# Kernel optimization log

Hardware: AMD Instinct MI355X
Metric: run time of the kernel (lower is better)

Reference implementation:

```python
import jax, jax.numpy as jnp
import numpy as np


def setup_inputs() -> dict:
    key = jax.random.key(0)
    k1, k2 = jax.random.split(key)
    B, C, T = 8, 64, 65536  # batch, channels, sequence length (power of 2)
    x = jax.random.normal(k1, (B, C, T), dtype=jnp.float32)
    h = jax.random.normal(k2, (B, C, T), dtype=jnp.float32)
    return {"x": x, "h": h}


def reference(x, h):
    """Causal (linear) convolution of x with kernel h via FFT, truncated to
    the input length — the math computed by FlashFFTConv. The original module
    casts the signal x to bfloat16 before the conv (kernel h stays fp32); we
    mimic that quantization, then compute the FFT in fp32."""
    T = x.shape[-1]
    n = 2 * T  # zero-pad to 2T so circular conv == linear causal conv on [0, T)
    xb = x.astype(jnp.bfloat16).astype(jnp.float32)  # bf16 quantization of signal
    X = jnp.fft.rfft(xb, n=n)          # (B, C, T+1) complex64
    H = jnp.fft.rfft(h, n=n)           # (B, C, T+1) complex64
    y = jnp.fft.irfft(X * H, n=n)[..., :T]  # causal output, same length as x
    return y.astype(jnp.float32)
```

## Files before the change

### kernel.cpp

```cpp
#include <hip/hip_runtime.h>
#include <hip/hip_bf16.h>
#include <hip/hip_fp16.h>
#include <math.h>


#define TLEN 65536
#define NFFT 131072
#define NN1 512
#define NN2 256

#define WFENCE() asm volatile("s_waitcnt lgkmcnt(0)" ::: "memory")

typedef float cpx __attribute__((ext_vector_type(2)));

static __device__ __forceinline__ cpx mkc(float a, float b) { cpx r; r.x = a; r.y = b; return r; }
static __device__ __forceinline__ cpx h2c(__half2 h) { float2 f = __half22float2(h); return mkc(f.x, f.y); }
static __device__ __forceinline__ __half2 c2h(cpx c) { return __float22half2_rn(make_float2(c.x, c.y)); }

static __device__ __forceinline__ cpx cadd(cpx a, cpx b) {
  cpx d; asm("v_pk_add_f32 %0, %1, %2" : "=v"(d) : "v"(a), "v"(b)); return d;
}
static __device__ __forceinline__ cpx csub(cpx a, cpx b) {
  cpx d; asm("v_pk_add_f32 %0, %1, %2 neg_lo:[0,1] neg_hi:[0,1]" : "=v"(d) : "v"(a), "v"(b)); return d;
}
static __device__ __forceinline__ cpx cscale(cpx a, cpx c) {
  cpx d; asm("v_pk_mul_f32 %0, %1, %2" : "=v"(d) : "v"(a), "v"(c)); return d;
}
static __device__ __forceinline__ cpx cmul(cpx a, cpx b) {
  cpx t, d;
  asm("v_pk_mul_f32 %0, %1, %2 op_sel:[0,0] op_sel_hi:[0,1]" : "=v"(t) : "v"(a), "v"(b));
  asm("v_pk_fma_f32 %0, %1, %2, %3 op_sel:[1,1,0] op_sel_hi:[1,0,1] neg_lo:[1,0,0]"
      : "=v"(d) : "v"(a), "v"(b), "v"(t));
  return d;
}
static __device__ __forceinline__ cpx cmulc(cpx a, cpx b) {
  cpx t, d;
  asm("v_pk_mul_f32 %0, %1, %2 op_sel:[0,0] op_sel_hi:[0,1]" : "=v"(t) : "v"(a), "v"(b));
  asm("v_pk_fma_f32 %0, %1, %2, %3 op_sel:[1,1,0] op_sel_hi:[1,0,1] neg_hi:[0,0,1]"
      : "=v"(d) : "v"(a), "v"(b), "v"(t));
  return d;
}
template <int S> static __device__ __forceinline__ cpx cmuli(cpx a) {
  cpx z = mkc(0.f, 0.f); cpx d;
  if constexpr (S == 1)
    asm("v_pk_add_f32 %0, %1, %2 op_sel:[1,0] op_sel_hi:[0,0] neg_lo:[1,0]" : "=v"(d) : "v"(a), "v"(z));
  else
    asm("v_pk_add_f32 %0, %1, %2 op_sel:[1,0] op_sel_hi:[0,0] neg_hi:[1,0]" : "=v"(d) : "v"(a), "v"(z));
  return d;
}
template <int S> static __device__ __forceinline__ cpx cw1(cpx d, cpx Cc) {
  cpx u;
  if constexpr (S == -1)
    asm("v_pk_add_f32 %0, %1, %1 op_sel:[0,1] op_sel_hi:[1,0] neg_hi:[0,1]" : "=v"(u) : "v"(d));
  else
    asm("v_pk_add_f32 %0, %1, %1 op_sel:[0,1] op_sel_hi:[0,1] neg_lo:[0,1]" : "=v"(u) : "v"(d));
  return cscale(u, Cc);
}
template <int S> static __device__ __forceinline__ cpx cw3(cpx d, cpx Cc) {
  cpx u;
  if constexpr (S == -1)
    asm("v_pk_add_f32 %0, %1, %1 op_sel:[1,0] op_sel_hi:[0,1] neg_lo:[0,1] neg_hi:[1,1]" : "=v"(u) : "v"(d));
  else
    asm("v_pk_add_f32 %0, %1, %1 op_sel:[0,1] op_sel_hi:[0,1] neg_lo:[1,1] neg_hi:[0,1]" : "=v"(u) : "v"(d));
  return cscale(u, Cc);
}

template <int S>
__device__ __forceinline__ void fft8(cpx v[8]) {
  cpx Cc; Cc.x = 0.70710678118654752f; Cc.y = 0.70710678118654752f;
  cpx b0 = cadd(v[0], v[4]), b4 = csub(v[0], v[4]);
  cpx b1 = cadd(v[1], v[5]), d1 = csub(v[1], v[5]);
  cpx b2 = cadd(v[2], v[6]), d2 = csub(v[2], v[6]);
  cpx b3 = cadd(v[3], v[7]), d3 = csub(v[3], v[7]);
  cpx b5 = cw1<S>(d1, Cc);
  cpx b6 = cmuli<S>(d2);
  cpx b7 = cw3<S>(d3, Cc);
  cpx c0 = cadd(b0, b2), c2 = csub(b0, b2);
  cpx c1 = cadd(b1, b3), e3 = csub(b1, b3);
  cpx c3 = cmuli<S>(e3);
  cpx c4 = cadd(b4, b6), c6 = csub(b4, b6);
  cpx c5 = cadd(b5, b7), e7 = csub(b5, b7);
  cpx c7 = cmuli<S>(e7);
  v[0] = cadd(c0, c1); v[4] = csub(c0, c1);
  v[2] = cadd(c2, c3); v[6] = csub(c2, c3);
  v[1] = cadd(c4, c5); v[5] = csub(c4, c5);
  v[3] = cadd(c6, c7); v[7] = csub(c6, c7);
}

template <int S>
__device__ __forceinline__ void fft4(cpx v[4]) {
  cpx t0 = cadd(v[0], v[2]), t1 = csub(v[0], v[2]);
  cpx t2 = cadd(v[1], v[3]), t3 = csub(v[1], v[3]);
  cpx it3 = cmuli<S>(t3);
  v[0] = cadd(t0, t2); v[2] = csub(t0, t2);
  v[1] = cadd(t1, it3); v[3] = csub(t1, it3);
}

__global__ void k_init_tw(cpx* __restrict__ tw) {
  int m = blockIdx.x * 256 + threadIdx.x;
  double ang = (double)m * (-2.0 * 3.14159265358979323846 / (double)NFFT);
  tw[m] = mkc((float)cos(ang), (float)sin(ang));
}

__global__ __launch_bounds__(256, 3) void k_fwd_inner(
    const float* __restrict__ x, const float* __restrict__ h,
    __half2* __restrict__ buf, const cpx* __restrict__ tw) {
  __shared__ __half2 tz[128 * 18];
  __shared__ cpx xch[4 * 512];
  __shared__ __half2 to[256 * 17];
  __shared__ cpx w256[256];
  const int tid = threadIdx.x;
  const int lane = tid & 63;
  const int wid = tid >> 6;
  const int s = blockIdx.x >> 5;
  const int n1b = (blockIdx.x & 31) * 16;
  w256[tid] = tw[tid * (NFFT / 256)];
  const float* xp = x + (size_t)s * TLEN;
  const float* hp = h + (size_t)s * TLEN;
  {
    int a = tid & 3, q = tid >> 2;
#pragma unroll
    for (int iter = 0; iter < 2; ++iter) {
      int n2 = q + 64 * iter;
      size_t gi = (size_t)(n1b + 4 * a) + (size_t)512 * n2;
      float4 xv = *(const float4*)(xp + gi);
      float4 hv = *(const float4*)(hp + gi);
      float xs[4] = {xv.x, xv.y, xv.z, xv.w};
      float hs[4] = {hv.x, hv.y, hv.z, hv.w};
#pragma unroll
      for (int c = 0; c < 4; ++c) {
        float xb = __bfloat162float(__float2bfloat16(xs[c]));
        tz[18 * n2 + 4 * a + c] = __float22half2_rn(make_float2(xb, hs[c]));
      }
    }
  }
  __syncthreads();
  cpx* X = xch + wid * 512;
  const int f = lane >> 5;
  const int l5 = lane & 31;
  const int fb = f * 256;
  const int hh = l5 >> 2, bb = l5 & 3;
#pragma unroll
  for (int p2 = 0; p2 < 2; ++p2) {
    const int n1l = 8 * p2 + 2 * wid + f;
    const int n1 = n1b + n1l;
    cpx tbase = tw[n1 * (hh + 8 * bb)];
    cpx tstep = tw[32 * n1];
    cpx v[8];
#pragma unroll
    for (int j = 0; j < 4; ++j) v[j] = h2c(tz[18 * (32 * j + l5) + n1l]);
#pragma unroll
    for (int j = 4; j < 8; ++j) v[j] = mkc(0.f, 0.f);
    fft8<-1>(v);
    { cpx w1 = w256[l5]; cpx pw = w1;
#pragma unroll
      for (int k0 = 1; k0 < 8; ++k0) { v[k0] = cmul(v[k0], pw); pw = cmul(pw, w1); } }
#pragma unroll
    for (int k0 = 0; k0 < 8; ++k0) X[fb + 32 * k0 + (l5 ^ (4 * k0))] = v[k0];
    WFENCE();
#pragma unroll
    for (int j2 = 0; j2 < 8; ++j2) v[j2] = X[fb + 32 * hh + ((4 * j2 + bb) ^ (4 * hh))];
    fft8<-1>(v);
    { cpx w1 = w256[8 * bb]; cpx pw = w1;
#pragma unroll
      for (int kp = 1; kp < 8; ++kp) { v[kp] = cmul(v[kp], pw); pw = cmul(pw, w1); } }
    WFENCE();
#pragma unroll
    for (int kp = 0; kp < 8; ++kp) {
      int cc = kp & 3, gg = kp >> 2;
      X[fb + 128 * gg + 32 * cc + 8 * (bb ^ cc) + hh] = v[kp];
    }
    WFENCE();
    cpx tstep2 = cmul(tstep, tstep);
#pragma unroll
    for (int g = 0; g < 2; ++g) {
      cpx u4[4];
#pragma unroll
      for (int t = 0; t < 4; ++t) u4[t] = X[fb + 128 * g + 32 * bb + 8 * (t ^ bb) + hh];
      fft4<-1>(u4);
      cpx wg = (g == 0) ? tbase : cmul(tbase, tstep);
#pragma unroll
      for (int k1q = 0; k1q < 4; ++k1q) {
        int k2 = hh + 8 * bb + 32 * g + 64 * k1q;
        cpx y = cmul(u4[k1q], wg);
        to[17 * k2 + n1l] = c2h(y);
        wg = cmul(wg, tstep2);
      }
    }
    WFENCE();
  }
  __syncthreads();
  {
    int c = tid & 3, q = tid >> 2;
#pragma unroll
    for (int iter = 0; iter < 4; ++iter) {
      int row = q + 64 * iter;
      __half2 h0 = to[17 * row + 4 * c + 0], h1 = to[17 * row + 4 * c + 1];
      __half2 h2v = to[17 * row + 4 * c + 2], h3 = to[17 * row + 4 * c + 3];
      int4 pk;
      pk.x = *(int*)&h0; pk.y = *(int*)&h1; pk.z = *(int*)&h2v; pk.w = *(int*)&h3;
      *(int4*)(buf + ((size_t)s * NN2 + row) * NN1 + n1b + 4 * c) = pk;
    }
  }
}

__global__ __launch_bounds__(256, 6) void k_mid(
    __half2* __restrict__ buf, const cpx* __restrict__ tw) {
  __shared__ cpx smem[4 * 576 + 512];
  cpx* w512 = smem + 4 * 576;
  const int tid = threadIdx.x;
  const int lane = tid & 63;
  const int wid = tid >> 6;
  const int s = blockIdx.x >> 6;
  const int pb = blockIdx.x & 63;
  for (int i = tid; i < 512; i += 256) w512[i] = tw[i * (NFFT / NN1)];
  const int p = 2 * pb + (wid >> 1);
  const int cidx = wid & 1;
  const int k2 = (p == 0) ? (cidx ? 128 : 0) : (cidx ? 256 - p : p);
  const int c = k2;
  const bool selfA = (p == 0 && cidx == 0);
  cpx* R = smem + wid * 576;
  cpx* PR = smem + ((p == 0) ? wid : (wid ^ 1)) * 576;
  __half2* colp = buf + ((size_t)s * NN2 + c) * NN1;

  const int jm = lane >> 3, mo = lane & 7;
  const int kbase = jm + 8 * mo;
  const float invN4 = 0.25f / (float)NFFT;
  cpx tbase = cscale(tw[kbase * k2], mkc(invN4, invN4));
  cpx tstep = tw[64 * k2];

  cpx v[8];
#pragma unroll
  for (int k = 0; k < 8; ++k) v[k] = h2c(colp[lane + 64 * k]);
  __syncthreads();

  fft8<-1>(v);
  { cpx w1 = w512[lane]; cpx pw = w1;
#pragma unroll
    for (int j = 1; j < 8; ++j) { v[j] = cmul(v[j], pw); pw = cmul(pw, w1); } }
#pragma unroll
  for (int j = 0; j < 8; ++j) R[64 * j + (lane ^ (8 * j))] = v[j];
  WFENCE();
#pragma unroll
  for (int m1 = 0; m1 < 8; ++m1) v[m1] = R[64 * jm + ((mo + 8 * m1) ^ (8 * jm))];
  fft8<-1>(v);
  { cpx w1 = w512[8 * mo]; cpx pw = w1;
#pragma unroll
    for (int r0 = 1; r0 < 8; ++r0) { v[r0] = cmul(v[r0], pw); pw = cmul(pw, w1); } }
  WFENCE();
#pragma unroll
  for (int r0 = 0; r0 < 8; ++r0) R[9 * (8 * jm + r0) + mo] = v[r0];
  WFENCE();
#pragma unroll
  for (int m0 = 0; m0 < 8; ++m0) v[m0] = R[9 * lane + m0];
  fft8<-1>(v);

  WFENCE();
#pragma unroll
  for (int r1 = 0; r1 < 8; ++r1) { int k = kbase + 64 * r1; R[k + (k >> 3)] = v[r1]; }
  __syncthreads();
  cpx z2[8];
#pragma unroll
  for (int r1 = 0; r1 < 8; ++r1) {
    int k = kbase + 64 * r1;
    int pk = selfA ? ((512 - k) & 511) : (511 - k);
    z2[r1] = PR[pk + (pk >> 3)];
  }
  __syncthreads();
#pragma unroll
  for (int r1 = 0; r1 < 8; ++r1) {
    cpx z1 = v[r1], q = z2[r1];
    cpx Xf2, Hf2;
    asm("v_pk_add_f32 %0, %1, %2 neg_hi:[0,1]" : "=v"(Xf2) : "v"(z1), "v"(q));
    asm("v_pk_add_f32 %0, %1, %2 op_sel:[1,1] op_sel_hi:[0,0] neg_hi:[1,0]" : "=v"(Hf2) : "v"(z1), "v"(q));
    v[r1] = cmul(Xf2, Hf2);
  }
#pragma unroll
  for (int r1 = 0; r1 < 8; ++r1) { int k = kbase + 64 * r1; R[k + (k >> 3)] = v[r1]; }
  WFENCE();
#pragma unroll
  for (int kk = 0; kk < 8; ++kk) { int ci = lane + 64 * kk; v[kk] = R[ci + (ci >> 3)]; }

  fft8<1>(v);
  { cpx w1 = w512[lane]; w1.y = -w1.y; cpx pw = w1;
#pragma unroll
    for (int j = 1; j < 8; ++j) { v[j] = cmul(v[j], pw); pw = cmul(pw, w1); } }
  WFENCE();
#pragma unroll
  for (int j = 0; j < 8; ++j) R[64 * j + (lane ^ (8 * j))] = v[j];
  WFENCE();
#pragma unroll
  for (int m1 = 0; m1 < 8; ++m1) v[m1] = R[64 * jm + ((mo + 8 * m1) ^ (8 * jm))];
  fft8<1>(v);
  { cpx w1 = w512[8 * mo]; w1.y = -w1.y; cpx pw = w1;
#pragma unroll
    for (int r0 = 1; r0 < 8; ++r0) { v[r0] = cmul(v[r0], pw); pw = cmul(pw, w1); } }
  WFENCE();
#pragma unroll
  for (int r0 = 0; r0 < 8; ++r0) R[9 * (8 * jm + r0) + mo] = v[r0];
  WFENCE();
#pragma unroll
  for (int m0 = 0; m0 < 8; ++m0) v[m0] = R[9 * lane + m0];
  fft8<1>(v);

  WFENCE();
#pragma unroll
  for (int r1 = 0; r1 < 8; ++r1) {
    int n1 = kbase + 64 * r1;
    cpx y = cmulc(v[r1], tbase);
    R[n1 + (n1 >> 3)] = y;
    tbase = cmul(tbase, tstep);
  }
  WFENCE();
#pragma unroll
  for (int u = 0; u < 8; ++u) {
    int ci = lane + 64 * u;
    colp[ci] = c2h(R[ci + (ci >> 3)]);
  }
}

__global__ __launch_bounds__(256, 3) void k_inv_outer(
    const __half2* __restrict__ buf, float* __restrict__ out,
    const cpx* __restrict__ tw) {
  __shared__ __half2 ti[16 * 257];
  __shared__ cpx xch[4 * 512];
  __shared__ float ty[128 * 17];
  __shared__ cpx w256[256];
  const int tid = threadIdx.x;
  const int lane = tid & 63;
  const int wid = tid >> 6;
  const int s = blockIdx.x >> 5;
  const int n1b = (blockIdx.x & 31) * 16;
  w256[tid] = tw[tid * (NFFT / 256)];
  {
    int c = tid & 3, q = tid >> 2;
#pragma unroll
    for (int iter = 0; iter < 4; ++iter) {
      int row = q + 64 * iter;
      int4 pk = *(const int4*)(buf + ((size_t)s * NN2 + row) * NN1 + n1b + 4 * c);
      __half2 hv[4];
      *(int*)&hv[0] = pk.x; *(int*)&hv[1] = pk.y; *(int*)&hv[2] = pk.z; *(int*)&hv[3] = pk.w;
#pragma unroll
      for (int j = 0; j < 4; ++j) ti[(4 * c + j) * 257 + row] = hv[j];
    }
  }
  __syncthreads();
  cpx* X = xch + wid * 512;
  const int f = lane >> 5;
  const int l5 = lane & 31;
  const int fb = f * 256;
  const int hh = l5 >> 2, bb = l5 & 3;
#pragma unroll
  for (int p2 = 0; p2 < 2; ++p2) {
    const int n1l = 8 * p2 + 2 * wid + f;
    cpx v2[2][4];
#pragma unroll
    for (int g = 0; g < 2; ++g)
#pragma unroll
      for (int k1q = 0; k1q < 4; ++k1q)
        v2[g][k1q] = h2c(ti[n1l * 257 + hh + 8 * bb + 32 * g + 64 * k1q]);
#pragma unroll
    for (int g = 0; g < 2; ++g) fft4<1>(v2[g]);
#pragma unroll
    for (int g = 0; g < 2; ++g)
#pragma unroll
      for (int t = 0; t < 4; ++t)
        X[fb + 128 * g + 32 * bb + 8 * (t ^ bb) + hh] = v2[g][t];
    WFENCE();
    cpx v[8];
#pragma unroll
    for (int kp = 0; kp < 8; ++kp) {
      int cc = kp & 3, gg = kp >> 2;
      v[kp] = X[fb + 128 * gg + 32 * cc + 8 * (bb ^ cc) + hh];
    }
    { cpx w1 = w256[8 * bb]; w1.y = -w1.y; cpx pw = w1;
#pragma unroll
      for (int kp = 1; kp < 8; ++kp) { v[kp] = cmul(v[kp], pw); pw = cmul(pw, w1); } }
    fft8<1>(v);
    WFENCE();
#pragma unroll
    for (int j2 = 0; j2 < 8; ++j2) X[fb + 32 * hh + ((4 * j2 + bb) ^ (4 * hh))] = v[j2];
    WFENCE();
#pragma unroll
    for (int k0 = 0; k0 < 8; ++k0) v[k0] = X[fb + 32 * k0 + (l5 ^ (4 * k0))];
    { cpx w1 = w256[l5]; w1.y = -w1.y; cpx pw = w1;
#pragma unroll
      for (int k0 = 1; k0 < 8; ++k0) { v[k0] = cmul(v[k0], pw); pw = cmul(pw, w1); } }
    fft8<1>(v);
#pragma unroll
    for (int j = 0; j < 4; ++j) ty[17 * (32 * j + l5) + n1l] = v[j].x;
    WFENCE();
  }
  __syncthreads();
  {
    int e = tid & 1, n2 = tid >> 1;
    float* op = out + (size_t)s * TLEN + (size_t)512 * n2 + n1b + 8 * e;
    float4 o0, o1;
    o0.x = ty[17 * n2 + 8 * e + 0]; o0.y = ty[17 * n2 + 8 * e + 1];
    o0.z = ty[17 * n2 + 8 * e + 2]; o0.w = ty[17 * n2 + 8 * e + 3];
    o1.x = ty[17 * n2 + 8 * e + 4]; o1.y = ty[17 * n2 + 8 * e + 5];
    o1.z = ty[17 * n2 + 8 * e + 6]; o1.w = ty[17 * n2 + 8 * e + 7];
    *(float4*)op = o0;
    *(float4*)(op + 4) = o1;
  }
}

extern "C" void kernel_launch(void* const* d_in, const int* in_sizes, int n_in,
                              void* d_out, int out_size, void* d_ws, size_t ws_size,
                              hipStream_t stream) {
  (void)n_in; (void)out_size; (void)ws_size;
  const float* x = (const float*)d_in[0];
  const float* h = (const float*)d_in[1];
  float* out = (float*)d_out;
  cpx* tw = (cpx*)d_ws;
  __half2* buf = (__half2*)((char*)d_ws + (size_t)(2 * 1024 * 1024));
  int seqs = in_sizes[0] / TLEN;
  k_init_tw<<<NFFT / 256, 256, 0, stream>>>(tw);
  k_fwd_inner<<<seqs * 32, 256, 0, stream>>>(x, h, buf, tw);
  k_mid<<<seqs * 64, 256, 0, stream>>>(buf, tw);
  k_inv_outer<<<seqs * 32, 256, 0, stream>>>(buf, out, tw);
}
```

Before: 698.8 us.

## Load twiddle powers directly from table, half-zero FFT8, pair columns per wave in mid

Twiddle factors are now read directly from the global table instead of being built by repeated complex multiplications from a shared-memory base, which removes the rounding drift of the chained products and the shared twiddle staging. The first forward radix-8 stage gets a specialised butterfly that skips work on the known-zero upper half. In k_mid each wave now handles both the column and its mirror column, so the Hermitian pairing happens inside the wave without block-wide barriers. The cost is more global twiddle loads (mostly cache hits), more registers per thread, a lower occupancy bound of 4 instead of 6, and half as many mid blocks.

After: 1.156 ms. +65.4%, slower.

```diff
diff --git a/kernel.cpp b/kernel.cpp
--- a/kernel.cpp
+++ b/kernel.cpp
@@ -88,6 +88,24 @@
 }
 
 template <int S>
+__device__ __forceinline__ void fft8h(cpx v[8]) {
+  cpx Cc; Cc.x = 0.70710678118654752f; Cc.y = 0.70710678118654752f;
+  cpx b5 = cw1<S>(v[1], Cc);
+  cpx b6 = cmuli<S>(v[2]);
+  cpx b7 = cw3<S>(v[3], Cc);
+  cpx c0 = cadd(v[0], v[2]), c2 = csub(v[0], v[2]);
+  cpx c1 = cadd(v[1], v[3]), e3 = csub(v[1], v[3]);
+  cpx c3 = cmuli<S>(e3);
+  cpx c4 = cadd(v[0], b6), c6 = csub(v[0], b6);
+  cpx c5 = cadd(b5, b7), e7 = csub(b5, b7);
+  cpx c7 = cmuli<S>(e7);
+  v[0] = cadd(c0, c1); v[4] = csub(c0, c1);
+  v[2] = cadd(c2, c3); v[6] = csub(c2, c3);
+  v[1] = cadd(c4, c5); v[5] = csub(c4, c5);
+  v[3] = cadd(c6, c7); v[7] = csub(c6, c7);
+}
+
+template <int S>
 __device__ __forceinline__ void fft4(cpx v[4]) {
   cpx t0 = cadd(v[0], v[2]), t1 = csub(v[0], v[2]);
   cpx t2 = cadd(v[1], v[3]), t3 = csub(v[1], v[3]);
@@ -108,13 +126,11 @@
   __shared__ __half2 tz[128 * 18];
   __shared__ cpx xch[4 * 512];
   __shared__ __half2 to[256 * 17];
-  __shared__ cpx w256[256];
   const int tid = threadIdx.x;
   const int lane = tid & 63;
   const int wid = tid >> 6;
   const int s = blockIdx.x >> 5;
   const int n1b = (blockIdx.x & 31) * 16;
-  w256[tid] = tw[tid * (NFFT / 256)];
   const float* xp = x + (size_t)s * TLEN;
   const float* hp = h + (size_t)s * TLEN;
   {
@@ -134,36 +150,35 @@
       }
     }
   }
-  __syncthreads();
   cpx* X = xch + wid * 512;
   const int f = lane >> 5;
   const int l5 = lane & 31;
   const int fb = f * 256;
   const int hh = l5 >> 2, bb = l5 & 3;
+  cpx pw1[7], pw2[7];
+#pragma unroll
+  for (int j = 1; j <= 7; ++j) pw1[j - 1] = tw[512 * l5 * j];
+#pragma unroll
+  for (int j = 1; j <= 7; ++j) pw2[j - 1] = tw[4096 * bb * j];
+  __syncthreads();
 #pragma unroll
   for (int p2 = 0; p2 < 2; ++p2) {
     const int n1l = 8 * p2 + 2 * wid + f;
     const int n1 = n1b + n1l;
-    cpx tbase = tw[n1 * (hh + 8 * bb)];
-    cpx tstep = tw[32 * n1];
     cpx v[8];
 #pragma unroll
     for (int j = 0; j < 4; ++j) v[j] = h2c(tz[18 * (32 * j + l5) + n1l]);
-#pragma unroll
-    for (int j = 4; j < 8; ++j) v[j] = mkc(0.f, 0.f);
-    fft8<-1>(v);
-    { cpx w1 = w256[l5]; cpx pw = w1;
-#pragma unroll
-      for (int k0 = 1; k0 < 8; ++k0) { v[k0] = cmul(v[k0], pw); pw = cmul(pw, w1); } }
+    fft8h<-1>(v);
+#pragma unroll
+    for (int k0 = 1; k0 < 8; ++k0) v[k0] = cmul(v[k0], pw1[k0 - 1]);
 #pragma unroll
     for (int k0 = 0; k0 < 8; ++k0) X[fb + 32 * k0 + (l5 ^ (4 * k0))] = v[k0];
     WFENCE();
 #pragma unroll
     for (int j2 = 0; j2 < 8; ++j2) v[j2] = X[fb + 32 * hh + ((4 * j2 + bb) ^ (4 * hh))];
     fft8<-1>(v);
-    { cpx w1 = w256[8 * bb]; cpx pw = w1;
-#pragma unroll
-      for (int kp = 1; kp < 8; ++kp) { v[kp] = cmul(v[kp], pw); pw = cmul(pw, w1); } }
+#pragma unroll
+    for (int kp = 1; kp < 8; ++kp) v[kp] = cmul(v[kp], pw2[kp - 1]);
     WFENCE();
 #pragma unroll
     for (int kp = 0; kp < 8; ++kp) {
@@ -171,20 +186,17 @@
       X[fb + 128 * gg + 32 * cc + 8 * (bb ^ cc) + hh] = v[kp];
     }
     WFENCE();
-    cpx tstep2 = cmul(tstep, tstep);
 #pragma unroll
     for (int g = 0; g < 2; ++g) {
       cpx u4[4];
 #pragma unroll
       for (int t = 0; t < 4; ++t) u4[t] = X[fb + 128 * g + 32 * bb + 8 * (t ^ bb) + hh];
       fft4<-1>(u4);
-      cpx wg = (g == 0) ? tbase : cmul(tbase, tstep);
 #pragma unroll
       for (int k1q = 0; k1q < 4; ++k1q) {
         int k2 = hh + 8 * bb + 32 * g + 64 * k1q;
-        cpx y = cmul(u4[k1q], wg);
+        cpx y = cmul(u4[k1q], tw[n1 * k2]);
         to[17 * k2 + n1l] = c2h(y);
-        wg = cmul(wg, tstep2);
       }
     }
     WFENCE();
@@ -204,118 +216,137 @@
   }
 }
 
-__global__ __launch_bounds__(256, 6) void k_mid(
+__global__ __launch_bounds__(256, 4) void k_mid(
     __half2* __restrict__ buf, const cpx* __restrict__ tw) {
-  __shared__ cpx smem[4 * 576 + 512];
-  cpx* w512 = smem + 4 * 576;
+  __shared__ cpx smem[4 * 1152];
   const int tid = threadIdx.x;
   const int lane = tid & 63;
   const int wid = tid >> 6;
-  const int s = blockIdx.x >> 6;
-  const int pb = blockIdx.x & 63;
-  for (int i = tid; i < 512; i += 256) w512[i] = tw[i * (NFFT / NN1)];
-  const int p = 2 * pb + (wid >> 1);
-  const int cidx = wid & 1;
-  const int k2 = (p == 0) ? (cidx ? 128 : 0) : (cidx ? 256 - p : p);
-  const int c = k2;
-  const bool selfA = (p == 0 && cidx == 0);
-  cpx* R = smem + wid * 576;
-  cpx* PR = smem + ((p == 0) ? wid : (wid ^ 1)) * 576;
-  __half2* colp = buf + ((size_t)s * NN2 + c) * NN1;
+  const int s = blockIdx.x >> 5;
+  const int p = (blockIdx.x & 31) * 4 + wid;
+  const bool self = (p == 0);
+  const int colA = self ? 0 : p;
+  const int colB = self ? 128 : 256 - p;
+  cpx* RA = smem + wid * 1152;
+  cpx* RB = RA + 576;
+  __half2* colpA = buf + ((size_t)s * NN2 + colA) * NN1;
+  __half2* colpB = buf + ((size_t)s * NN2 + colB) * NN1;
 
   const int jm = lane >> 3, mo = lane & 7;
   const int kbase = jm + 8 * mo;
+
+  cpx pA[7], pB[7];
+#pragma unroll
+  for (int j = 1; j <= 7; ++j) pA[j - 1] = tw[256 * lane * j];
+#pragma unroll
+  for (int j = 1; j <= 7; ++j) pB[j - 1] = tw[2048 * mo * j];
+
+  cpx va[8], vb[8];
+#pragma unroll
+  for (int k = 0; k < 8; ++k) va[k] = h2c(colpA[lane + 64 * k]);
+#pragma unroll
+  for (int k = 0; k < 8; ++k) vb[k] = h2c(colpB[lane + 64 * k]);
+
+  fft8<-1>(va); fft8<-1>(vb);
+#pragma unroll
+  for (int j = 1; j < 8; ++j) { va[j] = cmul(va[j], pA[j - 1]); vb[j] = cmul(vb[j], pA[j - 1]); }
+#pragma unroll
+  for (int j = 0; j < 8; ++j) { int a = 64 * j + (lane ^ (8 * j)); RA[a] = va[j]; RB[a] = vb[j]; }
+  WFENCE();
+#pragma unroll
+  for (int m1 = 0; m1 < 8; ++m1) { int a = 64 * jm + ((mo + 8 * m1) ^ (8 * jm)); va[m1] = RA[a]; vb[m1] = RB[a]; }
+  fft8<-1>(va); fft8<-1>(vb);
+#pragma unroll
+  for (int r0 = 1; r0 < 8; ++r0) { va[r0] = cmul(va[r0], pB[r0 - 1]); vb[r0] = cmul(vb[r0], pB[r0 - 1]); }
+  WFENCE();
+#pragma unroll
+  for (int r0 = 0; r0 < 8; ++r0) { int a = 9 * (8 * jm + r0) + mo; RA[a] = va[r0]; RB[a] = vb[r0]; }
+  WFENCE();
+#pragma unroll
+  for (int m0 = 0; m0 < 8; ++m0) { va[m0] = RA[9 * lane + m0]; vb[m0] = RB[9 * lane + m0]; }
+  fft8<-1>(va); fft8<-1>(vb);
+  WFENCE();
+#pragma unroll
+  for (int r1 = 0; r1 < 8; ++r1) { int k = kbase + 64 * r1; int a = k + (k >> 3); RA[a] = va[r1]; RB[a] = vb[r1]; }
+  WFENCE();
+  {
+    cpx q[8];
+#pragma unroll
+    for (int r1 = 0; r1 < 8; ++r1) {
+      int k = kbase + 64 * r1;
+      int pk = self ? ((512 - k) & 511) : (511 - k);
+      q[r1] = (self ? RA : RB)[pk + (pk >> 3)];
+    }
+#pragma unroll
+    for (int r1 = 0; r1 < 8; ++r1) {
+      cpx z1 = va[r1], qq = q[r1], Xf2, Hf2;
+      asm("v_pk_add_f32 %0, %1, %2 neg_hi:[0,1]" : "=v"(Xf2) : "v"(z1), "v"(qq));
+      asm("v_pk_add_f32 %0, %1, %2 op_sel:[1,1] op_sel_hi:[0,0] neg_hi:[1,0]" : "=v"(Hf2) : "v"(z1), "v"(qq));
+      va[r1] = cmul(Xf2, Hf2);
+    }
+  }
+  {
+    cpx q[8];
+#pragma unroll
+    for (int r1 = 0; r1 < 8; ++r1) {
+      int k = kbase + 64 * r1;
+      int pk = 511 - k;
+      q[r1] = (self ? RB : RA)[pk + (pk >> 3)];
+    }
+#pragma unroll
+    for (int r1 = 0; r1 < 8; ++r1) {
+      cpx z1 = vb[r1], qq = q[r1], Xf2, Hf2;
+      asm("v_pk_add_f32 %0, %1, %2 neg_hi:[0,1]" : "=v"(Xf2) : "v"(z1), "v"(qq));
+      asm("v_pk_add_f32 %0, %1, %2 op_sel:[1,1] op_sel_hi:[0,0] neg_hi:[1,0]" : "=v"(Hf2) : "v"(z1), "v"(qq));
+      vb[r1] = cmul(Xf2, Hf2);
+    }
+  }
+  WFENCE();
+#pragma unroll
+  for (int r1 = 0; r1 < 8; ++r1) { int k = kbase + 64 * r1; int a = k + (k >> 3); RA[a] = va[r1]; RB[a] = vb[r1]; }
+  WFENCE();
+#pragma unroll
+  for (int kk = 0; kk < 8; ++kk) { int ci = lane + 64 * kk; int a = ci + (ci >> 3); va[kk] = RA[a]; vb[kk] = RB[a]; }
+
+  fft8<1>(va); fft8<1>(vb);
+#pragma unroll
+  for (int j = 1; j < 8; ++j) { va[j] = cmulc(va[j], pA[j - 1]); vb[j] = cmulc(vb[j], pA[j - 1]); }
+  WFENCE();
+#pragma unroll
+  for (int j = 0; j < 8; ++j) { int a = 64 * j + (lane ^ (8 * j)); RA[a] = va[j]; RB[a] = vb[j]; }
+  WFENCE();
+#pragma unroll
+  for (int m1 = 0; m1 < 8; ++m1) { int a = 64 * jm + ((mo + 8 * m1) ^ (8 * jm)); va[m1] = RA[a]; vb[m1] = RB[a]; }
+  fft8<1>(va); fft8<1>(vb);
+#pragma unroll
+  for (int r0 = 1; r0 < 8; ++r0) { va[r0] = cmulc(va[r0], pB[r0 - 1]); vb[r0] = cmulc(vb[r0], pB[r0 - 1]); }
+  WFENCE();
+#pragma unroll
+  for (int r0 = 0; r0 < 8; ++r0) { int a = 9 * (8 * jm + r0) + mo; RA[a] = va[r0]; RB[a] = vb[r0]; }
+  WFENCE();
+#pragma unroll
+  for (int m0 = 0; m0 < 8; ++m0) { va[m0] = RA[9 * lane + m0]; vb[m0] = RB[9 * lane + m0]; }
+  fft8<1>(va); fft8<1>(vb);
+
   const float invN4 = 0.25f / (float)NFFT;
-  cpx tbase = cscale(tw[kbase * k2], mkc(invN4, invN4));
-  cpx tstep = tw[64 * k2];
-
-  cpx v[8];
-#pragma unroll
-  for (int k = 0; k < 8; ++k) v[k] = h2c(colp[lane + 64 * k]);
-  __syncthreads();
-
-  fft8<-1>(v);
-  { cpx w1 = w512[lane]; cpx pw = w1;
-#pragma unroll
-    for (int j = 1; j < 8; ++j) { v[j] = cmul(v[j], pw); pw = cmul(pw, w1); } }
-#pragma unroll
-  for (int j = 0; j < 8; ++j) R[64 * j + (lane ^ (8 * j))] = v[j];
-  WFENCE();
-#pragma unroll
-  for (int m1 = 0; m1 < 8; ++m1) v[m1] = R[64 * jm + ((mo + 8 * m1) ^ (8 * jm))];
-  fft8<-1>(v);
-  { cpx w1 = w512[8 * mo]; cpx pw = w1;
-#pragma unroll
-    for (int r0 = 1; r0 < 8; ++r0) { v[r0] = cmul(v[r0], pw); pw = cmul(pw, w1); } }
-  WFENCE();
-#pragma unroll
-  for (int r0 = 0; r0 < 8; ++r0) R[9 * (8 * jm + r0) + mo] = v[r0];
-  WFENCE();
-#pragma unroll
-  for (int m0 = 0; m0 < 8; ++m0) v[m0] = R[9 * lane + m0];
-  fft8<-1>(v);
-
-  WFENCE();
-#pragma unroll
-  for (int r1 = 0; r1 < 8; ++r1) { int k = kbase + 64 * r1; R[k + (k >> 3)] = v[r1]; }
-  __syncthreads();
-  cpx z2[8];
-#pragma unroll
-  for (int r1 = 0; r1 < 8; ++r1) {
-    int k = kbase + 64 * r1;
-    int pk = selfA ? ((512 - k) & 511) : (511 - k);
-    z2[r1] = PR[pk + (pk >> 3)];
-  }
-  __syncthreads();
-#pragma unroll
-  for (int r1 = 0; r1 < 8; ++r1) {
-    cpx z1 = v[r1], q = z2[r1];
-    cpx Xf2, Hf2;
-    asm("v_pk_add_f32 %0, %1, %2 neg_hi:[0,1]" : "=v"(Xf2) : "v"(z1), "v"(q));
-    asm("v_pk_add_f32 %0, %1, %2 op_sel:[1,1] op_sel_hi:[0,0] neg_hi:[1,0]" : "=v"(Hf2) : "v"(z1), "v"(q));
-    v[r1] = cmul(Xf2, Hf2);
-  }
-#pragma unroll
-  for (int r1 = 0; r1 < 8; ++r1) { int k = kbase + 64 * r1; R[k + (k >> 3)] = v[r1]; }
-  WFENCE();
-#pragma unroll
-  for (int kk = 0; kk < 8; ++kk) { int ci = lane + 64 * kk; v[kk] = R[ci + (ci >> 3)]; }
-
-  fft8<1>(v);
-  { cpx w1 = w512[lane]; w1.y = -w1.y; cpx pw = w1;
-#pragma unroll
-    for (int j = 1; j < 8; ++j) { v[j] = cmul(v[j], pw); pw = cmul(pw, w1); } }
-  WFENCE();
-#pragma unroll
-  for (int j = 0; j < 8; ++j) R[64 * j + (lane ^ (8 * j))] = v[j];
-  WFENCE();
-#pragma unroll
-  for (int m1 = 0; m1 < 8; ++m1) v[m1] = R[64 * jm + ((mo + 8 * m1) ^ (8 * jm))];
-  fft8<1>(v);
-  { cpx w1 = w512[8 * mo]; w1.y = -w1.y; cpx pw = w1;
-#pragma unroll
-    for (int r0 = 1; r0 < 8; ++r0) { v[r0] = cmul(v[r0], pw); pw = cmul(pw, w1); } }
-  WFENCE();
-#pragma unroll
-  for (int r0 = 0; r0 < 8; ++r0) R[9 * (8 * jm + r0) + mo] = v[r0];
-  WFENCE();
-#pragma unroll
-  for (int m0 = 0; m0 < 8; ++m0) v[m0] = R[9 * lane + m0];
-  fft8<1>(v);
-
+  const cpx invc = mkc(invN4, invN4);
   WFENCE();
 #pragma unroll
   for (int r1 = 0; r1 < 8; ++r1) {
     int n1 = kbase + 64 * r1;
-    cpx y = cmulc(v[r1], tbase);
-    R[n1 + (n1 >> 3)] = y;
-    tbase = cmul(tbase, tstep);
+    cpx tA = cscale(tw[n1 * colA], invc);
+    cpx tB = cscale(tw[n1 * colB], invc);
+    cpx yA = cmulc(va[r1], tA);
+    cpx yB = cmulc(vb[r1], tB);
+    int a = n1 + (n1 >> 3);
+    RA[a] = yA; RB[a] = yB;
   }
   WFENCE();
 #pragma unroll
   for (int u = 0; u < 8; ++u) {
-    int ci = lane + 64 * u;
-    colp[ci] = c2h(R[ci + (ci >> 3)]);
+    int ci = lane + 64 * u; int a = ci + (ci >> 3);
+    colpA[ci] = c2h(RA[a]);
+    colpB[ci] = c2h(RB[a]);
   }
 }
 
@@ -325,13 +356,11 @@
   __shared__ __half2 ti[16 * 257];
   __shared__ cpx xch[4 * 512];
   __shared__ float ty[128 * 17];
-  __shared__ cpx w256[256];
   const int tid = threadIdx.x;
   const int lane = tid & 63;
   const int wid = tid >> 6;
   const int s = blockIdx.x >> 5;
   const int n1b = (blockIdx.x & 31) * 16;
-  w256[tid] = tw[tid * (NFFT / 256)];
   {
     int c = tid & 3, q = tid >> 2;
 #pragma unroll
@@ -344,12 +373,17 @@
       for (int j = 0; j < 4; ++j) ti[(4 * c + j) * 257 + row] = hv[j];
     }
   }
-  __syncthreads();
   cpx* X = xch + wid * 512;
   const int f = lane >> 5;
   const int l5 = lane & 31;
   const int fb = f * 256;
   const int hh = l5 >> 2, bb = l5 & 3;
+  cpx pw1[7], pw2[7];
+#pragma unroll
+  for (int j = 1; j <= 7; ++j) pw1[j - 1] = tw[512 * l5 * j];
+#pragma unroll
+  for (int j = 1; j <= 7; ++j) pw2[j - 1] = tw[4096 * bb * j];
+  __syncthreads();
 #pragma unroll
   for (int p2 = 0; p2 < 2; ++p2) {
     const int n1l = 8 * p2 + 2 * wid + f;
@@ -373,9 +407,8 @@
       int cc = kp & 3, gg = kp >> 2;
       v[kp] = X[fb + 128 * gg + 32 * cc + 8 * (bb ^ cc) + hh];
     }
-    { cpx w1 = w256[8 * bb]; w1.y = -w1.y; cpx pw = w1;
-#pragma unroll
-      for (int kp = 1; kp < 8; ++kp) { v[kp] = cmul(v[kp], pw); pw = cmul(pw, w1); } }
+#pragma unroll
+    for (int kp = 1; kp < 8; ++kp) v[kp] = cmulc(v[kp], pw2[kp - 1]);
     fft8<1>(v);
     WFENCE();
 #pragma unroll
@@ -383,9 +416,8 @@
     WFENCE();
 #pragma unroll
     for (int k0 = 0; k0 < 8; ++k0) v[k0] = X[fb + 32 * k0 + (l5 ^ (4 * k0))];
-    { cpx w1 = w256[l5]; w1.y = -w1.y; cpx pw = w1;
-#pragma unroll
-      for (int k0 = 1; k0 < 8; ++k0) { v[k0] = cmul(v[k0], pw); pw = cmul(pw, w1); } }
+#pragma unroll
+    for (int k0 = 1; k0 < 8; ++k0) v[k0] = cmulc(v[k0], pw1[k0 - 1]);
     fft8<1>(v);
 #pragma unroll
     for (int j = 0; j < 4; ++j) ty[17 * (32 * j + l5) + n1l] = v[j].x;
@@ -417,6 +449,6 @@
   int seqs = in_sizes[0] / TLEN;
   k_init_tw<<<NFFT / 256, 256, 0, stream>>>(tw);
   k_fwd_inner<<<seqs * 32, 256, 0, stream>>>(x, h, buf, tw);
-  k_mid<<<seqs * 64, 256, 0, stream>>>(buf, tw);
+  k_mid<<<seqs * 32, 256, 0, stream>>>(buf, tw);
   k_inv_outer<<<seqs * 32, 256, 0, stream>>>(buf, out, tw);
 }
```

## Alias shared buffers, precompute twiddle powers in registers, raise occupancy bounds

Applied to the files above, without the earlier changes.

The input and output staging buffers in the forward and inverse outer kernels now share one shared-memory region, and the shared twiddle tables are dropped. Each thread instead reads its base twiddle from global memory and precomputes its powers in registers, and the launch-bound occupancy targets rise (3→4 and 6→7). The forward first radix-8 stage uses a half-input butterfly that skips the known zero-padded half, and the mid kernel's final store writes two half2 values at once. This trades lower LDS use and fewer instructions for more register pressure, an extra barrier from the aliasing, and slight twiddle-accuracy drift from the repeated multiplies.

Result: slower. 939.3 us (+34.4%).

```diff
diff --git a/kernel.cpp b/kernel.cpp
--- a/kernel.cpp
+++ b/kernel.cpp
@@ -88,6 +88,24 @@
 }
 
 template <int S>
+__device__ __forceinline__ void fft8h(cpx v[8]) {
+  cpx Cc; Cc.x = 0.70710678118654752f; Cc.y = 0.70710678118654752f;
+  cpx b5 = cw1<S>(v[1], Cc);
+  cpx b6 = cmuli<S>(v[2]);
+  cpx b7 = cw3<S>(v[3], Cc);
+  cpx c0 = cadd(v[0], v[2]), c2 = csub(v[0], v[2]);
+  cpx c1 = cadd(v[1], v[3]), e3 = csub(v[1], v[3]);
+  cpx c3 = cmuli<S>(e3);
+  cpx c4 = cadd(v[0], b6), c6 = csub(v[0], b6);
+  cpx c5 = cadd(b5, b7), e7 = csub(b5, b7);
+  cpx c7 = cmuli<S>(e7);
+  v[0] = cadd(c0, c1); v[4] = csub(c0, c1);
+  v[2] = cadd(c2, c3); v[6] = csub(c2, c3);
+  v[1] = cadd(c4, c5); v[5] = csub(c4, c5);
+  v[3] = cadd(c6, c7); v[7] = csub(c6, c7);
+}
+
+template <int S>
 __device__ __forceinline__ void fft4(cpx v[4]) {
   cpx t0 = cadd(v[0], v[2]), t1 = csub(v[0], v[2]);
   cpx t2 = cadd(v[1], v[3]), t3 = csub(v[1], v[3]);
@@ -102,19 +120,18 @@
   tw[m] = mkc((float)cos(ang), (float)sin(ang));
 }
 
-__global__ __launch_bounds__(256, 3) void k_fwd_inner(
+__global__ __launch_bounds__(256, 4) void k_fwd_inner(
     const float* __restrict__ x, const float* __restrict__ h,
     __half2* __restrict__ buf, const cpx* __restrict__ tw) {
-  __shared__ __half2 tz[128 * 18];
-  __shared__ cpx xch[4 * 512];
-  __shared__ __half2 to[256 * 17];
-  __shared__ cpx w256[256];
+  __shared__ __align__(16) char sraw[17408 + 16384];
+  __half2* tz = (__half2*)sraw;
+  __half2* to = (__half2*)sraw;
+  cpx* xch = (cpx*)(sraw + 17408);
   const int tid = threadIdx.x;
   const int lane = tid & 63;
   const int wid = tid >> 6;
   const int s = blockIdx.x >> 5;
   const int n1b = (blockIdx.x & 31) * 16;
-  w256[tid] = tw[tid * (NFFT / 256)];
   const float* xp = x + (size_t)s * TLEN;
   const float* hp = h + (size_t)s * TLEN;
   {
@@ -134,57 +151,69 @@
       }
     }
   }
-  __syncthreads();
   cpx* X = xch + wid * 512;
   const int f = lane >> 5;
   const int l5 = lane & 31;
   const int fb = f * 256;
   const int hh = l5 >> 2, bb = l5 & 3;
+  cpx pw1[7], pw2[7];
+  pw1[0] = tw[512 * l5];
+  pw2[0] = tw[4096 * bb];
+#pragma unroll
+  for (int j = 1; j < 7; ++j) pw1[j] = cmul(pw1[j - 1], pw1[0]);
+#pragma unroll
+  for (int j = 1; j < 7; ++j) pw2[j] = cmul(pw2[j - 1], pw2[0]);
+  __syncthreads();
+  cpx vin[2][4];
+#pragma unroll
+  for (int p2 = 0; p2 < 2; ++p2) {
+    const int n1l = 8 * p2 + 2 * wid + f;
+#pragma unroll
+    for (int j = 0; j < 4; ++j) vin[p2][j] = h2c(tz[18 * (32 * j + l5) + n1l]);
+  }
+  __syncthreads();
 #pragma unroll
   for (int p2 = 0; p2 < 2; ++p2) {
     const int n1l = 8 * p2 + 2 * wid + f;
     const int n1 = n1b + n1l;
-    cpx tbase = tw[n1 * (hh + 8 * bb)];
-    cpx tstep = tw[32 * n1];
+    const cpx wb = tw[n1 * (hh + 8 * bb)];
+    const cpx wst = tw[32 * n1];
     cpx v[8];
 #pragma unroll
-    for (int j = 0; j < 4; ++j) v[j] = h2c(tz[18 * (32 * j + l5) + n1l]);
-#pragma unroll
-    for (int j = 4; j < 8; ++j) v[j] = mkc(0.f, 0.f);
-    fft8<-1>(v);
-    { cpx w1 = w256[l5]; cpx pw = w1;
-#pragma unroll
-      for (int k0 = 1; k0 < 8; ++k0) { v[k0] = cmul(v[k0], pw); pw = cmul(pw, w1); } }
+    for (int j = 0; j < 4; ++j) v[j] = vin[p2][j];
+    fft8h<-1>(v);
+#pragma unroll
+    for (int k0 = 1; k0 < 8; ++k0) v[k0] = cmul(v[k0], pw1[k0 - 1]);
 #pragma unroll
     for (int k0 = 0; k0 < 8; ++k0) X[fb + 32 * k0 + (l5 ^ (4 * k0))] = v[k0];
     WFENCE();
 #pragma unroll
     for (int j2 = 0; j2 < 8; ++j2) v[j2] = X[fb + 32 * hh + ((4 * j2 + bb) ^ (4 * hh))];
     fft8<-1>(v);
-    { cpx w1 = w256[8 * bb]; cpx pw = w1;
-#pragma unroll
-      for (int kp = 1; kp < 8; ++kp) { v[kp] = cmul(v[kp], pw); pw = cmul(pw, w1); } }
+#pragma unroll
+    for (int kp = 1; kp < 8; ++kp) v[kp] = cmul(v[kp], pw2[kp - 1]);
     WFENCE();
 #pragma unroll
     for (int kp = 0; kp < 8; ++kp) {
       int cc = kp & 3, gg = kp >> 2;
       X[fb + 128 * gg + 32 * cc + 8 * (bb ^ cc) + hh] = v[kp];
     }
-    WFENCE();
-    cpx tstep2 = cmul(tstep, tstep);
+    cpx wg[8];
+    wg[0] = wb;
+#pragma unroll
+    for (int m = 1; m < 8; ++m) wg[m] = cmul(wg[m - 1], wst);
+    WFENCE();
 #pragma unroll
     for (int g = 0; g < 2; ++g) {
       cpx u4[4];
 #pragma unroll
       for (int t = 0; t < 4; ++t) u4[t] = X[fb + 128 * g + 32 * bb + 8 * (t ^ bb) + hh];
       fft4<-1>(u4);
-      cpx wg = (g == 0) ? tbase : cmul(tbase, tstep);
 #pragma unroll
       for (int k1q = 0; k1q < 4; ++k1q) {
         int k2 = hh + 8 * bb + 32 * g + 64 * k1q;
-        cpx y = cmul(u4[k1q], wg);
+        cpx y = cmul(u4[k1q], wg[g + 2 * k1q]);
         to[17 * k2 + n1l] = c2h(y);
-        wg = cmul(wg, tstep2);
       }
     }
     WFENCE();
@@ -204,49 +233,49 @@
   }
 }
 
-__global__ __launch_bounds__(256, 6) void k_mid(
+__global__ __launch_bounds__(256, 7) void k_mid(
     __half2* __restrict__ buf, const cpx* __restrict__ tw) {
-  __shared__ cpx smem[4 * 576 + 512];
-  cpx* w512 = smem + 4 * 576;
+  __shared__ cpx smem[4 * 576];
   const int tid = threadIdx.x;
   const int lane = tid & 63;
   const int wid = tid >> 6;
   const int s = blockIdx.x >> 6;
   const int pb = blockIdx.x & 63;
-  for (int i = tid; i < 512; i += 256) w512[i] = tw[i * (NFFT / NN1)];
   const int p = 2 * pb + (wid >> 1);
   const int cidx = wid & 1;
   const int k2 = (p == 0) ? (cidx ? 128 : 0) : (cidx ? 256 - p : p);
-  const int c = k2;
   const bool selfA = (p == 0 && cidx == 0);
   cpx* R = smem + wid * 576;
   cpx* PR = smem + ((p == 0) ? wid : (wid ^ 1)) * 576;
-  __half2* colp = buf + ((size_t)s * NN2 + c) * NN1;
+  __half2* colp = buf + ((size_t)s * NN2 + k2) * NN1;
 
   const int jm = lane >> 3, mo = lane & 7;
   const int kbase = jm + 8 * mo;
-  const float invN4 = 0.25f / (float)NFFT;
-  cpx tbase = cscale(tw[kbase * k2], mkc(invN4, invN4));
-  cpx tstep = tw[64 * k2];
 
   cpx v[8];
 #pragma unroll
   for (int k = 0; k < 8; ++k) v[k] = h2c(colp[lane + 64 * k]);
-  __syncthreads();
+
+  cpx pA[7];
+  pA[0] = tw[256 * lane];
+#pragma unroll
+  for (int j = 1; j < 7; ++j) pA[j] = cmul(pA[j - 1], pA[0]);
+  const cpx pB0 = tw[2048 * mo];
+  const cpx tbase0 = tw[kbase * k2];
+  const cpx tstep = tw[64 * k2];
 
   fft8<-1>(v);
-  { cpx w1 = w512[lane]; cpx pw = w1;
-#pragma unroll
-    for (int j = 1; j < 8; ++j) { v[j] = cmul(v[j], pw); pw = cmul(pw, w1); } }
+#pragma unroll
+  for (int j = 1; j < 8; ++j) v[j] = cmul(v[j], pA[j - 1]);
 #pragma unroll
   for (int j = 0; j < 8; ++j) R[64 * j + (lane ^ (8 * j))] = v[j];
   WFENCE();
 #pragma unroll
   for (int m1 = 0; m1 < 8; ++m1) v[m1] = R[64 * jm + ((mo + 8 * m1) ^ (8 * jm))];
   fft8<-1>(v);
-  { cpx w1 = w512[8 * mo]; cpx pw = w1;
-#pragma unroll
-    for (int r0 = 1; r0 < 8; ++r0) { v[r0] = cmul(v[r0], pw); pw = cmul(pw, w1); } }
+  { cpx pw = pB0;
+#pragma unroll
+    for (int r0 = 1; r0 < 8; ++r0) { v[r0] = cmul(v[r0], pw); if (r0 < 7) pw = cmul(pw, pB0); } }
   WFENCE();
 #pragma unroll
   for (int r0 = 0; r0 < 8; ++r0) R[9 * (8 * jm + r0) + mo] = v[r0];
@@ -269,10 +298,9 @@
   __syncthreads();
 #pragma unroll
   for (int r1 = 0; r1 < 8; ++r1) {
-    cpx z1 = v[r1], q = z2[r1];
-    cpx Xf2, Hf2;
-    asm("v_pk_add_f32 %0, %1, %2 neg_hi:[0,1]" : "=v"(Xf2) : "v"(z1), "v"(q));
-    asm("v_pk_add_f32 %0, %1, %2 op_sel:[1,1] op_sel_hi:[0,0] neg_hi:[1,0]" : "=v"(Hf2) : "v"(z1), "v"(q));
+    cpx z1 = v[r1], qq = z2[r1], Xf2, Hf2;
+    asm("v_pk_add_f32 %0, %1, %2 neg_hi:[0,1]" : "=v"(Xf2) : "v"(z1), "v"(qq));
+    asm("v_pk_add_f32 %0, %1, %2 op_sel:[1,1] op_sel_hi:[0,0] neg_hi:[1,0]" : "=v"(Hf2) : "v"(z1), "v"(qq));
     v[r1] = cmul(Xf2, Hf2);
   }
 #pragma unroll
@@ -282,9 +310,8 @@
   for (int kk = 0; kk < 8; ++kk) { int ci = lane + 64 * kk; v[kk] = R[ci + (ci >> 3)]; }
 
   fft8<1>(v);
-  { cpx w1 = w512[lane]; w1.y = -w1.y; cpx pw = w1;
-#pragma unroll
-    for (int j = 1; j < 8; ++j) { v[j] = cmul(v[j], pw); pw = cmul(pw, w1); } }
+#pragma unroll
+  for (int j = 1; j < 8; ++j) v[j] = cmulc(v[j], pA[j - 1]);
   WFENCE();
 #pragma unroll
   for (int j = 0; j < 8; ++j) R[64 * j + (lane ^ (8 * j))] = v[j];
@@ -292,9 +319,9 @@
 #pragma unroll
   for (int m1 = 0; m1 < 8; ++m1) v[m1] = R[64 * jm + ((mo + 8 * m1) ^ (8 * jm))];
   fft8<1>(v);
-  { cpx w1 = w512[8 * mo]; w1.y = -w1.y; cpx pw = w1;
-#pragma unroll
-    for (int r0 = 1; r0 < 8; ++r0) { v[r0] = cmul(v[r0], pw); pw = cmul(pw, w1); } }
+  { cpx pw = pB0;
+#pragma unroll
+    for (int r0 = 1; r0 < 8; ++r0) { v[r0] = cmulc(v[r0], pw); if (r0 < 7) pw = cmul(pw, pB0); } }
   WFENCE();
 #pragma unroll
   for (int r0 = 0; r0 < 8; ++r0) R[9 * (8 * jm + r0) + mo] = v[r0];
@@ -303,35 +330,38 @@
   for (int m0 = 0; m0 < 8; ++m0) v[m0] = R[9 * lane + m0];
   fft8<1>(v);
 
+  const float invN4 = 0.25f / (float)NFFT;
+  cpx tA = cscale(tbase0, mkc(invN4, invN4));
   WFENCE();
 #pragma unroll
   for (int r1 = 0; r1 < 8; ++r1) {
     int n1 = kbase + 64 * r1;
-    cpx y = cmulc(v[r1], tbase);
-    R[n1 + (n1 >> 3)] = y;
-    tbase = cmul(tbase, tstep);
-  }
-  WFENCE();
-#pragma unroll
-  for (int u = 0; u < 8; ++u) {
-    int ci = lane + 64 * u;
-    colp[ci] = c2h(R[ci + (ci >> 3)]);
-  }
-}
-
-__global__ __launch_bounds__(256, 3) void k_inv_outer(
+    R[n1 + (n1 >> 3)] = cmulc(v[r1], tA);
+    if (r1 < 7) tA = cmul(tA, tstep);
+  }
+  WFENCE();
+#pragma unroll
+  for (int u = 0; u < 4; ++u) {
+    int ci = 2 * lane + 128 * u;
+    int a0 = ci + (ci >> 3);
+    __half2 q0 = c2h(R[a0]), q1 = c2h(R[a0 + 1]);
+    int2 pk; pk.x = *(int*)&q0; pk.y = *(int*)&q1;
+    *(int2*)(colp + ci) = pk;
+  }
+}
+
+__global__ __launch_bounds__(256, 4) void k_inv_outer(
     const __half2* __restrict__ buf, float* __restrict__ out,
     const cpx* __restrict__ tw) {
-  __shared__ __half2 ti[16 * 257];
-  __shared__ cpx xch[4 * 512];
-  __shared__ float ty[128 * 17];
-  __shared__ cpx w256[256];
+  __shared__ __align__(16) char sraw[16448 + 16384];
+  __half2* ti = (__half2*)sraw;
+  float* ty = (float*)sraw;
+  cpx* xch = (cpx*)(sraw + 16448);
   const int tid = threadIdx.x;
   const int lane = tid & 63;
   const int wid = tid >> 6;
   const int s = blockIdx.x >> 5;
   const int n1b = (blockIdx.x & 31) * 16;
-  w256[tid] = tw[tid * (NFFT / 256)];
   {
     int c = tid & 3, q = tid >> 2;
 #pragma unroll
@@ -344,12 +374,30 @@
       for (int j = 0; j < 4; ++j) ti[(4 * c + j) * 257 + row] = hv[j];
     }
   }
-  __syncthreads();
   cpx* X = xch + wid * 512;
   const int f = lane >> 5;
   const int l5 = lane & 31;
   const int fb = f * 256;
   const int hh = l5 >> 2, bb = l5 & 3;
+  cpx pw1[7], pw2[7];
+  pw1[0] = tw[512 * l5];
+  pw2[0] = tw[4096 * bb];
+#pragma unroll
+  for (int j = 1; j < 7; ++j) pw1[j] = cmul(pw1[j - 1], pw1[0]);
+#pragma unroll
+  for (int j = 1; j < 7; ++j) pw2[j] = cmul(pw2[j - 1], pw2[0]);
+  __syncthreads();
+  cpx vin[2][2][4];
+#pragma unroll
+  for (int p2 = 0; p2 < 2; ++p2) {
+    const int n1l = 8 * p2 + 2 * wid + f;
+#pragma unroll
+    for (int g = 0; g < 2; ++g)
+#pragma unroll
+      for (int k1q = 0; k1q < 4; ++k1q)
+        vin[p2][g][k1q] = h2c(ti[n1l * 257 + hh + 8 * bb + 32 * g + 64 * k1q]);
+  }
+  __syncthreads();
 #pragma unroll
   for (int p2 = 0; p2 < 2; ++p2) {
     const int n1l = 8 * p2 + 2 * wid + f;
@@ -357,8 +405,7 @@
 #pragma unroll
     for (int g = 0; g < 2; ++g)
 #pragma unroll
-      for (int k1q = 0; k1q < 4; ++k1q)
-        v2[g][k1q] = h2c(ti[n1l * 257 + hh + 8 * bb + 32 * g + 64 * k1q]);
+      for (int k1q = 0; k1q < 4; ++k1q) v2[g][k1q] = vin[p2][g][k1q];
 #pragma unroll
     for (int g = 0; g < 2; ++g) fft4<1>(v2[g]);
 #pragma unroll
@@ -373,9 +420,8 @@
       int cc = kp & 3, gg = kp >> 2;
       v[kp] = X[fb + 128 * gg + 32 * cc + 8 * (bb ^ cc) + hh];
     }
-    { cpx w1 = w256[8 * bb]; w1.y = -w1.y; cpx pw = w1;
-#pragma unroll
-      for (int kp = 1; kp < 8; ++kp) { v[kp] = cmul(v[kp], pw); pw = cmul(pw, w1); } }
+#pragma unroll
+    for (int kp = 1; kp < 8; ++kp) v[kp] = cmulc(v[kp], pw2[kp - 1]);
     fft8<1>(v);
     WFENCE();
 #pragma unroll
@@ -383,9 +429,8 @@
     WFENCE();
 #pragma unroll
     for (int k0 = 0; k0 < 8; ++k0) v[k0] = X[fb + 32 * k0 + (l5 ^ (4 * k0))];
-    { cpx w1 = w256[l5]; w1.y = -w1.y; cpx pw = w1;
-#pragma unroll
-      for (int k0 = 1; k0 < 8; ++k0) { v[k0] = cmul(v[k0], pw); pw = cmul(pw, w1); } }
+#pragma unroll
+    for (int k0 = 1; k0 < 8; ++k0) v[k0] = cmulc(v[k0], pw1[k0 - 1]);
     fft8<1>(v);
 #pragma unroll
     for (int j = 0; j < 4; ++j) ty[17 * (32 * j + l5) + n1l] = v[j].x;
```
